# Performance work log

Measured on AMD Instinct MI355X. Metric: run time of the kernel, lower is better.

The kernel has to match this reference:

```python
import jax, jax.numpy as jnp
import numpy as np

EMBED_DIM = 1536
NUM_HEADS = 12
HEAD_DIM = EMBED_DIM // NUM_HEADS  # 128
SEQ = 2048
EPS = 1e-5


def rms_norm(x, w):
    # x: (..., HEAD_DIM)
    var = jnp.mean(jnp.square(x), axis=-1, keepdims=True)
    return x * jax.lax.rsqrt(var + EPS) * w


def apply_rotary(x, cos, sin):
    # x: (b, s, h, d); cos/sin: (s, d/2) -> broadcast (1, s, 1, d/2)
    d2 = cos.shape[-1]
    c = cos[None, :, None, :]
    s_ = sin[None, :, None, :]
    x1, x2 = x[..., :d2], x[..., d2:]
    return jnp.concatenate([x1 * c - x2 * s_, x2 * c + x1 * s_], axis=-1)


def setup_inputs() -> dict:
    key = jax.random.key(0)
    ks = jax.random.split(key, 10)
    x = jax.random.normal(ks[0], (SEQ, 1, EMBED_DIM), dtype=jnp.float32)
    cu_seqlens = jnp.array([0, SEQ // 2, SEQ], dtype=jnp.int32)
    # rotary tables for positions 0..SEQ-1, rotary dim = HEAD_DIM
    inv_freq = 1.0 / (10000.0 ** (jnp.arange(0, HEAD_DIM, 2, dtype=jnp.float32) / HEAD_DIM))
    pos = jnp.arange(SEQ, dtype=jnp.float32)
    freqs = pos[:, None] * inv_freq[None, :]  # (s, d/2)
    rotary_pos_emb_cos = jnp.cos(freqs)
    rotary_pos_emb_sin = jnp.sin(freqs)
    scale = 0.02
    w_qkv = jax.random.normal(ks[1], (EMBED_DIM, 3 * EMBED_DIM), dtype=jnp.float32) * scale
    b_qkv = jnp.zeros((3 * EMBED_DIM,), dtype=jnp.float32)
    q_norm_w = jnp.ones((HEAD_DIM,), dtype=jnp.float32)
    k_norm_w = jnp.ones((HEAD_DIM,), dtype=jnp.float32)
    w_proj = jax.random.normal(ks[2], (EMBED_DIM, EMBED_DIM), dtype=jnp.float32) * scale
    b_proj = jnp.zeros((EMBED_DIM,), dtype=jnp.float32)
    return {
        'x': x, 'cu_seqlens': cu_seqlens,
        'rotary_pos_emb_cos': rotary_pos_emb_cos, 'rotary_pos_emb_sin': rotary_pos_emb_sin,
        'w_qkv': w_qkv, 'b_qkv': b_qkv, 'q_norm_w': q_norm_w, 'k_norm_w': k_norm_w,
        'w_proj': w_proj, 'b_proj': b_proj,
    }


def reference(x, cu_seqlens, rotary_pos_emb_cos, rotary_pos_emb_sin,
              w_qkv, b_qkv, q_norm_w, k_norm_w, w_proj, b_proj):
    s, b, e = x.shape
    h, d = NUM_HEADS, HEAD_DIM
    qkv = jnp.einsum('sbe,ef->sbf', x, w_qkv) + b_qkv  # (s, b, 3e)
    q, k, v = jnp.split(qkv, 3, axis=2)
    q = q.reshape(s, b, h, d)
    k = k.reshape(s, b, h, d)
    v = v.reshape(s, b, h, d)
    # per-head RMSNorm on q/k
    q = rms_norm(q, q_norm_w)
    k = rms_norm(k, k_norm_w)
    # (s, b, h, d) -> (b, s, h, d)
    q = jnp.transpose(q, (1, 0, 2, 3))
    k = jnp.transpose(k, (1, 0, 2, 3))
    v = jnp.transpose(v, (1, 0, 2, 3))
    q = apply_rotary(q, rotary_pos_emb_cos, rotary_pos_emb_sin)
    k = apply_rotary(k, rotary_pos_emb_cos, rotary_pos_emb_sin)
    # varlen (block-diagonal, non-causal) attention via segment mask
    pos = jnp.arange(s)
    seg = jnp.searchsorted(cu_seqlens[1:], pos, side='right')  # (s,)
    mask = seg[:, None] == seg[None, :]  # (s, s)
    scale = d ** -0.5
    scores = jnp.einsum('bqhd,bkhd->bhqk', q, k) * scale  # (b, h, s, s)
    scores = jnp.where(mask[None, None, :, :], scores, jnp.finfo(scores.dtype).min)
    attn = jax.nn.softmax(scores, axis=-1)
    ctx = jnp.einsum('bhqk,bkhd->bqhd', attn, v)  # (b, s, h, d)
    # (b, s, h, d) -> (s, b, h*d)
    ctx = jnp.transpose(ctx, (1, 0, 2, 3)).reshape(s, b, h * d)
    out = jnp.einsum('sbe,ef->sbf', ctx, w_proj) + b_proj
    return out
```

## Files before the change

### kernel.cpp

```cpp
#include <hip/hip_runtime.h>
#include <hip/hip_bf16.h>
#include <stdint.h>

#define S_LEN 2048
#define EMB   1536
#define NH    12
#define HD    128
#define N3    4608
#define RMS_EPS 1e-5f
#define ATTN_SCALE 0.08838834764831845f

typedef short short8_t __attribute__((ext_vector_type(8)));
typedef float f32x4    __attribute__((ext_vector_type(4)));

typedef __attribute__((address_space(1))) const void g1_void;
typedef __attribute__((address_space(3))) void l3_void;

__device__ __forceinline__ void gload_lds16(const void* g, void* l) {
  __builtin_amdgcn_global_load_lds((g1_void*)g, (l3_void*)l, 16, 0, 0);
}

__device__ __forceinline__ short f2bf(float f) {
  union { float f; unsigned u; } v; v.f = f;
  unsigned r = (v.u + 0x7FFFu + ((v.u >> 16) & 1u)) >> 16;
  return (short)(r & 0xFFFFu);
}
__device__ __forceinline__ float bf2f(short s) {
  union { unsigned u; float f; } v; v.u = ((unsigned)(unsigned short)s) << 16;
  return v.f;
}

__global__ __launch_bounds__(256) void k_cvt_bf16(const float* __restrict__ in,
                                                  short* __restrict__ out, int n) {
  int i = (blockIdx.x * 256 + threadIdx.x) * 4;
  if (i + 3 < n) {
    float4 v = *(const float4*)(in + i);
    short4 o;
    o.x = f2bf(v.x); o.y = f2bf(v.y); o.z = f2bf(v.z); o.w = f2bf(v.w);
    *(short4*)(out + i) = o;
  }
}

__global__ __launch_bounds__(256) void k_transpose_cvt(const float* __restrict__ W,
                                                       short* __restrict__ Wt,
                                                       int K, int N) {
  __shared__ float t[32][33];
  int n0 = blockIdx.x * 32, k0 = blockIdx.y * 32;
  int tx = threadIdx.x, ty = threadIdx.y;
#pragma unroll
  for (int r = 0; r < 4; ++r) {
    int k = ty + r * 8;
    t[k][tx] = W[(size_t)(k0 + k) * N + n0 + tx];
  }
  __syncthreads();
#pragma unroll
  for (int r = 0; r < 4; ++r) {
    int j = ty + r * 8;
    Wt[(size_t)(n0 + j) * K + k0 + tx] = f2bf(t[tx][j]);
  }
}

template<bool OBF>
__global__ __launch_bounds__(256) void k_gemm_v2(const short* __restrict__ A,
                                                 const short* __restrict__ Bt,
                                                 const float* __restrict__ bias,
                                                 void* __restrict__ Cv,
                                                 int M, int N, int K) {
  __shared__ short lds[2][2][128 * 64];
  const int tid = threadIdx.x;
  const int lane = tid & 63, wid = tid >> 6;
  const int wr = (wid >> 1) * 64, wc = (wid & 1) * 64;
  const int bn = blockIdx.x * 128, bm = blockIdx.y * 128;
  const int lr = lane & 15, lg = lane >> 4;
  const int swz = (lr & 7) << 4;

  const int srow = lane >> 3;
  const int skc  = ((lane & 7) ^ srow) * 8;

  f32x4 acc[4][4] = {};
  const int nk = K >> 6;

#pragma unroll
  for (int it = 0; it < 4; ++it) {
    int seg = wid * 4 + it;
    int row = seg * 8 + srow;
    gload_lds16(A  + (size_t)(bm + row) * K + skc, &lds[0][0][seg * 512]);
    gload_lds16(Bt + (size_t)(bn + row) * K + skc, &lds[0][1][seg * 512]);
  }
  __syncthreads();

  int cur = 0;
  for (int t = 0; t < nk; ++t) {
    if (t + 1 < nk) {
      const int kt = (t + 1) << 6;
#pragma unroll
      for (int it = 0; it < 4; ++it) {
        int seg = wid * 4 + it;
        int row = seg * 8 + srow;
        gload_lds16(A  + (size_t)(bm + row) * K + kt + skc, &lds[cur ^ 1][0][seg * 512]);
        gload_lds16(Bt + (size_t)(bn + row) * K + kt + skc, &lds[cur ^ 1][1][seg * 512]);
      }
    }
    const char* baseA = (const char*)&lds[cur][0][0];
    const char* baseB = (const char*)&lds[cur][1][0];
#pragma unroll
    for (int kk = 0; kk < 2; ++kk) {
      short8_t af[4], bfr[4];
#pragma unroll
      for (int m = 0; m < 4; ++m) {
        int row = wr + m * 16 + lr;
        af[m] = *(const short8_t*)(baseA + ((row * 128 + kk * 64 + lg * 16) ^ swz));
      }
#pragma unroll
      for (int n = 0; n < 4; ++n) {
        int row = wc + n * 16 + lr;
        bfr[n] = *(const short8_t*)(baseB + ((row * 128 + kk * 64 + lg * 16) ^ swz));
      }
#pragma unroll
      for (int m = 0; m < 4; ++m)
#pragma unroll
        for (int n = 0; n < 4; ++n)
          acc[m][n] = __builtin_amdgcn_mfma_f32_16x16x32_bf16(af[m], bfr[n], acc[m][n], 0, 0, 0);
    }
    __syncthreads();
    cur ^= 1;
  }

#pragma unroll
  for (int m = 0; m < 4; ++m)
#pragma unroll
    for (int n = 0; n < 4; ++n) {
      int col = bn + wc + n * 16 + lr;
      float bv = bias[col];
#pragma unroll
      for (int r = 0; r < 4; ++r) {
        int row = bm + wr + m * 16 + lg * 4 + r;
        float v = acc[m][n][r] + bv;
        if (OBF) ((short*)Cv)[(size_t)row * N + col] = f2bf(v);
        else     ((float*)Cv)[(size_t)row * N + col] = v;
      }
    }
}

__global__ __launch_bounds__(256) void k_post(const short* __restrict__ qkv,
                                              const float* __restrict__ cosv,
                                              const float* __restrict__ sinv,
                                              const float* __restrict__ qw,
                                              const float* __restrict__ kw,
                                              short* __restrict__ qb,
                                              short* __restrict__ kb,
                                              short* __restrict__ vt) {
  __shared__ short ldsv[64 * 130];
  const int h = blockIdx.x, s0 = blockIdx.y * 64;
  const int t = threadIdx.x;
  const int r = t >> 2, j = t & 3;
  const int s = s0 + r;
  const size_t rowbase = (size_t)s * N3 + h * HD;

  {
    const short* vp = qkv + rowbase + 2 * EMB + j * 32;
#pragma unroll
    for (int i4 = 0; i4 < 4; ++i4)
      *(short8_t*)&ldsv[r * 130 + j * 32 + i4 * 8] = *(const short8_t*)(vp + i4 * 8);
  }

#pragma unroll
  for (int qk = 0; qk < 2; ++qk) {
    const short* p = qkv + rowbase + qk * EMB + j * 32;
    const float* w = qk ? kw : qw;
    float v[32];
#pragma unroll
    for (int i4 = 0; i4 < 4; ++i4) {
      short8_t x = *(const short8_t*)(p + i4 * 8);
#pragma unroll
      for (int e = 0; e < 8; ++e) v[i4 * 8 + e] = bf2f(x[e]);
    }
    float ss = 0.f;
#pragma unroll
    for (int i = 0; i < 32; ++i) ss += v[i] * v[i];
    ss += __shfl_xor(ss, 1);
    ss += __shfl_xor(ss, 2);
    float rsq = rsqrtf(ss * (1.0f / HD) + RMS_EPS);
#pragma unroll
    for (int i = 0; i < 32; ++i) v[i] = v[i] * rsq * w[j * 32 + i];
    const float* cp = cosv + (size_t)s * 64 + (j & 1) * 32;
    const float* sp = sinv + (size_t)s * 64 + (j & 1) * 32;
    short out[32];
#pragma unroll
    for (int i = 0; i < 32; ++i) {
      float part = __shfl_xor(v[i], 2);
      float c = cp[i], sn = sp[i];
      float o = (j < 2) ? (v[i] * c - part * sn) : (v[i] * c + part * sn);
      out[i] = f2bf(o);
    }
    short* dst = (qk ? kb : qb) + ((size_t)h * S_LEN + s) * HD + j * 32;
#pragma unroll
    for (int i4 = 0; i4 < 4; ++i4) {
      short8_t o8;
#pragma unroll
      for (int e = 0; e < 8; ++e) o8[e] = out[i4 * 8 + e];
      *(short8_t*)(dst + i4 * 8) = o8;
    }
  }

  __syncthreads();
  const int sl = t & 63, wv = t >> 6;
#pragma unroll
  for (int it = 0; it < 32; ++it) {
    int d = it * 4 + wv;
    vt[((size_t)h * HD + d) * S_LEN + s0 + sl] = ldsv[sl * 130 + d];
  }
}

__global__ __launch_bounds__(256) void k_attn(const short* __restrict__ qb,
                                              const short* __restrict__ kb,
                                              const short* __restrict__ vt,
                                              const int* __restrict__ cu, int nseg,
                                              short* __restrict__ ctx) {
  __shared__ short ldsK[64 * 128];
  __shared__ short ldsV[128 * 64];
  __shared__ short ldsP[4 * 16 * 64];

  const int h = blockIdx.x, qt = blockIdx.y;
  const int q0 = qt * 64;
  const int tid = threadIdx.x, l = tid & 63, w = tid >> 6;
  const int lr = l & 15, lg = l >> 4;

  int rows[4], rs[4], re[4];
  float m[4], lsum[4];
#pragma unroll
  for (int r = 0; r < 4; ++r) {
    int row = q0 + w * 16 + lg * 4 + r;
    rows[r] = row;
    int seg = 0;
    for (int i = 1; i <= nseg; ++i) if (row >= cu[i]) seg = i;
    rs[r] = (seg == 0) ? 0 : cu[seg];
    re[r] = (seg < nseg) ? cu[seg + 1] : S_LEN;
    m[r] = -INFINITY;
    lsum[r] = 0.f;
  }

  int seg0 = 0, seg1 = 0;
  for (int i = 1; i <= nseg; ++i) {
    if (q0 >= cu[i]) seg0 = i;
    if (q0 + 63 >= cu[i]) seg1 = i;
  }
  const int ks = (seg0 == 0) ? 0 : cu[seg0];
  const int ke = (seg1 < nseg) ? cu[seg1 + 1] : S_LEN;
  const int kt0 = (ks >> 6) << 6;

  short8_t qf[4];
  {
    int srow = q0 + w * 16 + lr;
    const short* qp = qb + ((size_t)h * S_LEN + srow) * HD;
#pragma unroll
    for (int kk = 0; kk < 4; ++kk)
      qf[kk] = *(const short8_t*)(qp + kk * 32 + lg * 8);
  }

  f32x4 cacc[8] = {};

  for (int kt = kt0; kt < ke; kt += 64) {
    __syncthreads();
#pragma unroll
    for (int it = 0; it < 4; ++it) {
      int c = it * 256 + tid;
      int row = c >> 4, cc = c & 15;
      short8_t v = *(const short8_t*)&kb[((size_t)h * S_LEN + kt + row) * HD + cc * 8];
      int byte = row * 256 + cc * 16;
      byte ^= (row & 7) << 4;
      *(short8_t*)((char*)ldsK + byte) = v;
    }
#pragma unroll
    for (int it = 0; it < 4; ++it) {
      int c = it * 256 + tid;
      int d = c >> 3, cc = c & 7;
      short8_t v = *(const short8_t*)&vt[((size_t)h * HD + d) * S_LEN + kt + cc * 8];
      int byte = d * 128 + cc * 16;
      byte ^= (d & 7) << 4;
      *(short8_t*)((char*)ldsV + byte) = v;
    }
    __syncthreads();

    f32x4 sacc[4] = {};
#pragma unroll
    for (int n = 0; n < 4; ++n) {
#pragma unroll
      for (int kk = 0; kk < 4; ++kk) {
        int row = n * 16 + lr;
        int byte = row * 256 + (kk * 32 + lg * 8) * 2;
        byte ^= (row & 7) << 4;
        short8_t kf = *(const short8_t*)((const char*)ldsK + byte);
        sacc[n] = __builtin_amdgcn_mfma_f32_16x16x32_bf16(qf[kk], kf, sacc[n], 0, 0, 0);
      }
    }

    float sv[4][4];
#pragma unroll
    for (int n = 0; n < 4; ++n) {
      int key = kt + n * 16 + lr;
#pragma unroll
      for (int r = 0; r < 4; ++r) {
        float x = sacc[n][r] * ATTN_SCALE;
        sv[n][r] = (key >= rs[r] && key < re[r]) ? x : -1e30f;
      }
    }
    float alpha[4];
#pragma unroll
    for (int r = 0; r < 4; ++r) {
      float tm = fmaxf(fmaxf(sv[0][r], sv[1][r]), fmaxf(sv[2][r], sv[3][r]));
#pragma unroll
      for (int off = 1; off < 16; off <<= 1) tm = fmaxf(tm, __shfl_xor(tm, off));
      float mn = fmaxf(m[r], tm);
      alpha[r] = __expf(m[r] - mn);
      m[r] = mn;
      float ls = 0.f;
#pragma unroll
      for (int n = 0; n < 4; ++n) {
        float p = __expf(sv[n][r] - mn);
        sv[n][r] = p;
        ls += p;
      }
#pragma unroll
      for (int off = 1; off < 16; off <<= 1) ls += __shfl_xor(ls, off);
      lsum[r] = lsum[r] * alpha[r] + ls;
    }
#pragma unroll
    for (int n = 0; n < 8; ++n)
#pragma unroll
      for (int r = 0; r < 4; ++r) cacc[n][r] *= alpha[r];

#pragma unroll
    for (int n = 0; n < 4; ++n)
#pragma unroll
      for (int r = 0; r < 4; ++r) {
        int prow = lg * 4 + r;
        int pcol = n * 16 + lr;
        int byte = prow * 128 + pcol * 2;
        byte ^= (prow & 7) << 4;
        *(short*)((char*)ldsP + w * 2048 + byte) = f2bf(sv[n][r]);
      }
    __syncthreads();

#pragma unroll
    for (int kk = 0; kk < 2; ++kk) {
      int byteP = lr * 128 + (kk * 32 + lg * 8) * 2;
      byteP ^= (lr & 7) << 4;
      short8_t pf = *(const short8_t*)((const char*)ldsP + w * 2048 + byteP);
#pragma unroll
      for (int n = 0; n < 8; ++n) {
        int d = n * 16 + lr;
        int byteV = d * 128 + (kk * 32 + lg * 8) * 2;
        byteV ^= (d & 7) << 4;
        short8_t vf = *(const short8_t*)((const char*)ldsV + byteV);
        cacc[n] = __builtin_amdgcn_mfma_f32_16x16x32_bf16(pf, vf, cacc[n], 0, 0, 0);
      }
    }
  }

#pragma unroll
  for (int r = 0; r < 4; ++r) {
    float inv = 1.0f / lsum[r];
#pragma unroll
    for (int n = 0; n < 8; ++n) {
      float v = cacc[n][r] * inv;
      ctx[(size_t)rows[r] * EMB + h * HD + n * 16 + lr] = f2bf(v);
    }
  }
}

extern "C" void kernel_launch(void* const* d_in, const int* in_sizes, int n_in,
                              void* d_out, int out_size, void* d_ws, size_t ws_size,
                              hipStream_t stream) {
  const float* x      = (const float*)d_in[0];
  const int*   cu     = (const int*)d_in[1];
  const float* cosv   = (const float*)d_in[2];
  const float* sinv   = (const float*)d_in[3];
  const float* w_qkv  = (const float*)d_in[4];
  const float* b_qkv  = (const float*)d_in[5];
  const float* q_norm = (const float*)d_in[6];
  const float* k_norm = (const float*)d_in[7];
  const float* w_proj = (const float*)d_in[8];
  const float* b_proj = (const float*)d_in[9];
  const int nseg = in_sizes[1] - 1;

  char* ws = (char*)d_ws;
  short* xb     = (short*)(ws);
  short* wqkvT  = (short*)(ws + 6291456);
  short* wprojT = (short*)(ws + 20447232);
  short* qkv16  = (short*)(ws + 25165824);
  short* qb     = (short*)(ws + 44040192);
  short* kb     = (short*)(ws + 50331648);
  short* vt     = (short*)(ws + 56623104);
  short* ctxb   = (short*)(ws + 62914560);

  k_cvt_bf16<<<(S_LEN * EMB) / 1024, 256, 0, stream>>>(x, xb, S_LEN * EMB);
  k_transpose_cvt<<<dim3(N3 / 32, EMB / 32), dim3(32, 8), 0, stream>>>(w_qkv, wqkvT, EMB, N3);
  k_transpose_cvt<<<dim3(EMB / 32, EMB / 32), dim3(32, 8), 0, stream>>>(w_proj, wprojT, EMB, EMB);
  k_gemm_v2<true><<<dim3(N3 / 128, S_LEN / 128), 256, 0, stream>>>(xb, wqkvT, b_qkv, qkv16, S_LEN, N3, EMB);
  k_post<<<dim3(NH, S_LEN / 64), 256, 0, stream>>>(qkv16, cosv, sinv, q_norm, k_norm, qb, kb, vt);
  k_attn<<<dim3(NH, S_LEN / 64), 256, 0, stream>>>(qb, kb, vt, cu, nseg, ctxb);
  k_gemm_v2<false><<<dim3(EMB / 128, S_LEN / 128), 256, 0, stream>>>(ctxb, wprojT, b_proj, (float*)d_out, S_LEN, EMB, EMB);
}
```

Measured before the change: 150.6 us.

## Split attention KV range across three blocks and merge with combine kernel

```diff
diff --git a/kernel.cpp b/kernel.cpp
--- a/kernel.cpp
+++ b/kernel.cpp
@@ -9,6 +9,7 @@
 #define N3    4608
 #define RMS_EPS 1e-5f
 #define ATTN_SCALE 0.08838834764831845f
+#define SPLIT 3
 
 typedef short short8_t __attribute__((ext_vector_type(8)));
 typedef float f32x4    __attribute__((ext_vector_type(4)));
@@ -216,22 +217,22 @@
                                               const short* __restrict__ kb,
                                               const short* __restrict__ vt,
                                               const int* __restrict__ cu, int nseg,
-                                              short* __restrict__ ctx) {
+                                              short* __restrict__ Opart,
+                                              float* __restrict__ mlpart) {
   __shared__ short ldsK[64 * 128];
   __shared__ short ldsV[128 * 64];
   __shared__ short ldsP[4 * 16 * 64];
 
-  const int h = blockIdx.x, qt = blockIdx.y;
+  const int h = blockIdx.x, qt = blockIdx.y, p = blockIdx.z;
   const int q0 = qt * 64;
   const int tid = threadIdx.x, l = tid & 63, w = tid >> 6;
   const int lr = l & 15, lg = l >> 4;
 
-  int rows[4], rs[4], re[4];
+  int rs[4], re[4];
   float m[4], lsum[4];
 #pragma unroll
   for (int r = 0; r < 4; ++r) {
     int row = q0 + w * 16 + lg * 4 + r;
-    rows[r] = row;
     int seg = 0;
     for (int i = 1; i <= nseg; ++i) if (row >= cu[i]) seg = i;
     rs[r] = (seg == 0) ? 0 : cu[seg];
@@ -248,6 +249,10 @@
   const int ks = (seg0 == 0) ? 0 : cu[seg0];
   const int ke = (seg1 < nseg) ? cu[seg1 + 1] : S_LEN;
   const int kt0 = (ks >> 6) << 6;
+  const int nt = (ke - kt0 + 63) >> 6;
+  const int tpb = (nt + SPLIT - 1) / SPLIT;
+  const int tb0 = p * tpb;
+  const int tb1 = (tb0 + tpb < nt) ? tb0 + tpb : nt;
 
   short8_t qf[4];
   {
@@ -260,7 +265,8 @@
 
   f32x4 cacc[8] = {};
 
-  for (int kt = kt0; kt < ke; kt += 64) {
+  for (int ti = tb0; ti < tb1; ++ti) {
+    const int kt = kt0 + ti * 64;
     __syncthreads();
 #pragma unroll
     for (int it = 0; it < 4; ++it) {
@@ -317,9 +323,9 @@
       float ls = 0.f;
 #pragma unroll
       for (int n = 0; n < 4; ++n) {
-        float p = __expf(sv[n][r] - mn);
-        sv[n][r] = p;
-        ls += p;
+        float pv = __expf(sv[n][r] - mn);
+        sv[n][r] = pv;
+        ls += pv;
       }
 #pragma unroll
       for (int off = 1; off < 16; off <<= 1) ls += __shfl_xor(ls, off);
@@ -358,14 +364,68 @@
     }
   }
 
+  const int b = (h * 32 + qt) * SPLIT + p;
 #pragma unroll
   for (int r = 0; r < 4; ++r) {
-    float inv = 1.0f / lsum[r];
-#pragma unroll
-    for (int n = 0; n < 8; ++n) {
-      float v = cacc[n][r] * inv;
-      ctx[(size_t)rows[r] * EMB + h * HD + n * 16 + lr] = f2bf(v);
-    }
+    int qrow = w * 16 + lg * 4 + r;
+#pragma unroll
+    for (int n = 0; n < 8; ++n)
+      Opart[(size_t)b * 8192 + qrow * 128 + n * 16 + lr] = f2bf(cacc[n][r]);
+  }
+  if (lr == 0) {
+#pragma unroll
+    for (int r = 0; r < 4; ++r) {
+      int qrow = w * 16 + lg * 4 + r;
+      mlpart[(size_t)b * 128 + qrow] = m[r];
+      mlpart[(size_t)b * 128 + 64 + qrow] = lsum[r];
+    }
+  }
+}
+
+__global__ __launch_bounds__(256) void k_combine(const short* __restrict__ Opart,
+                                                 const float* __restrict__ ml,
+                                                 short* __restrict__ ctx) {
+  const int h = blockIdx.x, qt = blockIdx.y, t = threadIdx.x;
+  const int r = t >> 2, j = t & 3;
+  const int b0 = (h * 32 + qt) * SPLIT;
+
+  float mp[SPLIT], lp[SPLIT], wp[SPLIT];
+  float M = -INFINITY;
+#pragma unroll
+  for (int p = 0; p < SPLIT; ++p) {
+    mp[p] = ml[(size_t)(b0 + p) * 128 + r];
+    lp[p] = ml[(size_t)(b0 + p) * 128 + 64 + r];
+    M = fmaxf(M, mp[p]);
+  }
+  float L = 0.f;
+#pragma unroll
+  for (int p = 0; p < SPLIT; ++p) {
+    wp[p] = __expf(mp[p] - M);
+    L += lp[p] * wp[p];
+  }
+  const float inv = 1.0f / L;
+
+  float acc[32];
+#pragma unroll
+  for (int i = 0; i < 32; ++i) acc[i] = 0.f;
+#pragma unroll
+  for (int p = 0; p < SPLIT; ++p) {
+    const short* src = Opart + (size_t)(b0 + p) * 8192 + r * 128 + j * 32;
+#pragma unroll
+    for (int i4 = 0; i4 < 4; ++i4) {
+      short8_t v = *(const short8_t*)(src + i4 * 8);
+#pragma unroll
+      for (int e = 0; e < 8; ++e) acc[i4 * 8 + e] += wp[p] * bf2f(v[e]);
+    }
+  }
+
+  short* dst = ctx + (size_t)(qt * 64 + r) * EMB + h * HD + j * 32;
+#pragma unroll
+  for (int i4 = 0; i4 < 4; ++i4) {
+    short8_t o8;
+#pragma unroll
+    for (int e = 0; e < 8; ++e) o8[e] = f2bf(acc[i4 * 8 + e] * inv);
+    *(short8_t*)(dst + i4 * 8) = o8;
   }
 }
 
@@ -393,12 +453,15 @@
   short* kb     = (short*)(ws + 50331648);
   short* vt     = (short*)(ws + 56623104);
   short* ctxb   = (short*)(ws + 62914560);
+  short* Opart  = qkv16;
+  float* mlpart = (float*)ws;
 
   k_cvt_bf16<<<(S_LEN * EMB) / 1024, 256, 0, stream>>>(x, xb, S_LEN * EMB);
   k_transpose_cvt<<<dim3(N3 / 32, EMB / 32), dim3(32, 8), 0, stream>>>(w_qkv, wqkvT, EMB, N3);
   k_transpose_cvt<<<dim3(EMB / 32, EMB / 32), dim3(32, 8), 0, stream>>>(w_proj, wprojT, EMB, EMB);
   k_gemm_v2<true><<<dim3(N3 / 128, S_LEN / 128), 256, 0, stream>>>(xb, wqkvT, b_qkv, qkv16, S_LEN, N3, EMB);
   k_post<<<dim3(NH, S_LEN / 64), 256, 0, stream>>>(qkv16, cosv, sinv, q_norm, k_norm, qb, kb, vt);
-  k_attn<<<dim3(NH, S_LEN / 64), 256, 0, stream>>>(qb, kb, vt, cu, nseg, ctxb);
+  k_attn<<<dim3(NH, S_LEN / 64, SPLIT), 256, 0, stream>>>(qb, kb, vt, cu, nseg, Opart, mlpart);
+  k_combine<<<dim3(NH, S_LEN / 64), 256, 0, stream>>>(Opart, mlpart, ctxb);
   k_gemm_v2<false><<<dim3(EMB / 128, S_LEN / 128), 256, 0, stream>>>(ctxb, wprojT, b_proj, (float*)d_out, S_LEN, EMB, EMB);
 }
```

Result: no change. 153.0 us (+1.6%).
